# Performance work log

Hardware: AMD Instinct MI355X
Metric: run time of the kernel (lower is better)

Reference implementation:

```python
import jax, jax.numpy as jnp
import numpy as np
from jax import lax

# sign binarization to {-1,+1} with straight-through estimator (standard BNN binarizePM1)
@jax.custom_vjp
def binarize(x):
    return jnp.where(x >= 0, 1.0, -1.0).astype(x.dtype)

def _bin_fwd(x):
    return binarize(x), None

def _bin_bwd(_, g):
    return (g,)  # straight-through

binarize.defvjp(_bin_fwd, _bin_bwd)

def conv2d(x, w, b):
    # NCHW, OIHW, 3x3, stride 1, pad 1
    y = lax.conv_general_dilated(x, w, window_strides=(1, 1), padding=((1, 1), (1, 1)),
                                 dimension_numbers=('NCHW', 'OIHW', 'NCHW'))
    return y + b[None, :, None, None]

def maxpool2(x):
    return lax.reduce_window(x, -jnp.inf, lax.max, (1, 1, 2, 2), (1, 1, 2, 2), 'VALID')

def bn(x, gamma, beta, mean, var, eps=1e-5):
    # inference-mode batchnorm; broadcasts over channel axis 1 (4D) or feature axis 1 (2D)
    if x.ndim == 4:
        shp = (1, -1, 1, 1)
    else:
        shp = (1, -1)
    inv = gamma * lax.rsqrt(var + eps)
    return x * inv.reshape(shp) + (beta - mean * inv).reshape(shp)

def setup_inputs() -> dict:
    key = jax.random.key(0)
    ks = jax.random.split(key, 16)
    B = 4096
    d = {}
    d['x'] = jax.random.normal(ks[0], (B, 1, 28, 28), jnp.float32)
    d['conv1_w'] = jax.random.normal(ks[1], (64, 1, 3, 3), jnp.float32) * 0.1
    d['conv1_b'] = jax.random.normal(ks[2], (64,), jnp.float32) * 0.01
    d['conv2_w'] = jax.random.normal(ks[3], (64, 64, 3, 3), jnp.float32) * 0.05
    d['conv2_b'] = jax.random.normal(ks[4], (64,), jnp.float32) * 0.01
    d['fc1_w'] = jax.random.normal(ks[5], (2048, 7 * 7 * 64), jnp.float32) * 0.02
    d['fc1_b'] = jax.random.normal(ks[6], (2048,), jnp.float32) * 0.01
    d['fc2_w'] = jax.random.normal(ks[7], (10, 2048), jnp.float32) * 0.02
    d['fc2_b'] = jax.random.normal(ks[8], (10,), jnp.float32) * 0.01
    for i, (name, c) in enumerate([('bn1', 64), ('bn2', 64), ('bn3', 2048)]):
        d[name + '_gamma'] = jnp.ones((c,), jnp.float32)
        d[name + '_beta'] = jnp.zeros((c,), jnp.float32)
        d[name + '_mean'] = jax.random.normal(ks[9 + i], (c,), jnp.float32) * 0.1
        d[name + '_var'] = jax.random.uniform(ks[12 + i], (c,), jnp.float32, 0.5, 1.5)
    d['scale'] = jnp.array([1e-5], jnp.float32)
    return d

def reference(x, conv1_w, conv1_b, conv2_w, conv2_b, fc1_w, fc1_b, fc2_w, fc2_b,
              bn1_gamma, bn1_beta, bn1_mean, bn1_var,
              bn2_gamma, bn2_beta, bn2_mean, bn2_var,
              bn3_gamma, bn3_beta, bn3_mean, bn3_var, scale):
    h = conv2d(x, binarize(conv1_w), conv1_b)          # [B,64,28,28]
    h = maxpool2(h)                                    # [B,64,14,14]
    h = bn(h, bn1_gamma, bn1_beta, bn1_mean, bn1_var)
    h = jnp.clip(h, -1.0, 1.0)                         # hardtanh
    h = binarize(h)                                    # qact1
    h = conv2d(h, binarize(conv2_w), conv2_b)          # [B,64,14,14]
    h = maxpool2(h)                                    # [B,64,7,7]
    h = bn(h, bn2_gamma, bn2_beta, bn2_mean, bn2_var)
    h = jnp.clip(h, -1.0, 1.0)
    h = binarize(h)
    h = h.reshape(h.shape[0], -1)                      # [B,3136]
    h = h @ binarize(fc1_w).T + fc1_b                  # [B,2048]
    h = bn(h, bn3_gamma, bn3_beta, bn3_mean, bn3_var)
    h = jnp.clip(h, -1.0, 1.0)
    h = binarize(h)
    h = h @ binarize(fc2_w).T + fc2_b                  # [B,10]
    return h * scale
```

## Files before the change

### kernel.cpp

```cpp
#include <hip/hip_runtime.h>
#include <stdint.h>

typedef unsigned long long ULL;

__global__ __launch_bounds__(256) void prep_small(const float* __restrict__ w1,
        const float* __restrict__ w2, const float* __restrict__ fc2w,
        float* __restrict__ sgn1, ULL* __restrict__ wb2, ULL* __restrict__ wbf2) {
    int wave = threadIdx.x >> 6, lane = threadIdx.x & 63;
    int W = blockIdx.x * 4 + wave;
    if (W < 576) {
        int co = W / 9, tap = W - co * 9;
        ULL wd = __ballot(w2[(co * 64 + lane) * 9 + tap] >= 0.f);
        if (lane == 0) wb2[W] = wd;
    } else if (W < 896) {
        int idx = W - 576;
        int n = idx >> 5, k = idx & 31;
        ULL wd = __ballot(fc2w[n * 2048 + k * 64 + lane] >= 0.f);
        if (lane == 0) wbf2[idx] = wd;
    } else if (W < 905) {
        int i = (W - 896) * 64 + lane;
        if (i < 576) sgn1[i] = (w1[i] >= 0.f) ? 1.f : -1.f;
    }
}

__global__ __launch_bounds__(256) void prep_pack_fc1(const float* __restrict__ fc1w,
                                                     ULL* __restrict__ wbT) {
    __shared__ float rows[4 * 3136];
    int t = threadIdx.x;
    const float* src = fc1w + (size_t)blockIdx.x * 4 * 3136;
    for (int i = t; i < 4 * 3136; i += 256) rows[i] = src[i];
    __syncthreads();
    int wave = t >> 6, lane = t & 63;
    int n = blockIdx.x * 4 + wave;
    const float* r = rows + wave * 3136 + lane * 49;
    for (int p = 0; p < 49; ++p) {
        ULL wd = __ballot(r[p] >= 0.f);
        if (lane == 0) wbT[p * 2048 + n] = wd;
    }
}

__global__ __launch_bounds__(448, 4) void k1_conv1(const float* __restrict__ x,
        const float* __restrict__ sgn1, const float* __restrict__ b1,
        const float* __restrict__ g, const float* __restrict__ be,
        const float* __restrict__ mu, const float* __restrict__ va,
        ULL* __restrict__ qact1) {
    __shared__ float limg[30 * 30];
    int b = blockIdx.x, t = threadIdx.x;
    int wave = t >> 6, lane = t & 63;
    for (int i = t; i < 900; i += 448) limg[i] = 0.f;
    __syncthreads();
    const float* xb = x + (size_t)b * 784;
    for (int i = t; i < 784; i += 448) {
        int y = i / 28, xx = i - y * 28;
        limg[(xx + 1) * 30 + (y + 1)] = xb[i];
    }
    float w[9];
    #pragma unroll
    for (int k = 0; k < 9; ++k) w[k] = sgn1[lane * 9 + k];
    double iv = (double)g[lane] / sqrt((double)va[lane] + 1e-5);
    double cd = (double)be[lane] - (double)mu[lane] * iv;
    double bd = (double)b1[lane];
    __syncthreads();

    #pragma unroll
    for (int rr = 0; rr < 2; ++rr) {
        int py = wave + rr * 7;
        const float* base = &limg[2 * py];
        #pragma unroll
        for (int px = 0; px < 14; ++px) {
            float a00 = 0.f, a01 = 0.f, a10 = 0.f, a11 = 0.f;
            #pragma unroll
            for (int ky = 0; ky < 3; ++ky) {
                #pragma unroll
                for (int kx = 0; kx < 3; ++kx) {
                    float sv = w[ky * 3 + kx];
                    a00 = fmaf(base[(2 * px + kx)     * 30 + ky],     sv, a00);
                    a01 = fmaf(base[(2 * px + kx + 1) * 30 + ky],     sv, a01);
                    a10 = fmaf(base[(2 * px + kx)     * 30 + ky + 1], sv, a10);
                    a11 = fmaf(base[(2 * px + kx + 1) * 30 + ky + 1], sv, a11);
                }
            }
            float m = fmaxf(fmaxf(a00, a01), fmaxf(a10, a11));
            double v  = (double)m + bd;
            double tt = v * iv + cd;
            ULL word = __ballot(tt >= 0.0);
            if (lane == 0) qact1[(size_t)b * 196 + py * 14 + px] = word;
        }
    }
}

__global__ __launch_bounds__(448, 4) void k2_conv2(const ULL* __restrict__ qact1,
        const ULL* __restrict__ wb2, const float* __restrict__ b2,
        const float* __restrict__ g, const float* __restrict__ be,
        const float* __restrict__ mu, const float* __restrict__ va,
        ULL* __restrict__ qact2) {
    __shared__ ULL ap[16][16];
    int b = blockIdx.x, t = threadIdx.x;
    int pr = t >> 6, lane = t & 63;
    if (t < 256) ((ULL*)ap)[t] = 0ULL;
    __syncthreads();
    if (t < 196) ap[1 + t / 14][1 + t % 14] = qact1[(size_t)b * 196 + t];

    ULL wk[9];
    #pragma unroll
    for (int k = 0; k < 9; ++k) wk[k] = wb2[lane * 9 + k];
    int pw[9];
    #pragma unroll
    for (int k = 0; k < 9; ++k) pw[k] = 64 - 2 * (int)__popcll(wk[k]);

    double iv   = (double)g[lane] / sqrt((double)va[lane] + 1e-5);
    double cc   = (double)be[lane] - (double)mu[lane] * iv;
    double bias = (double)b2[lane];
    int am, thr;
    if (iv > 0.0) {
        double t0 = -cc / iv - bias;
        int c = (t0 < -590.0) ? -590 : (t0 > 590.0 ? 590 : (int)floor(t0) - 2);
        if (c < -590) c = -590;
        while (c <= 590 && !(((double)c + bias) * iv + cc >= 0.0)) ++c;
        am = 1; thr = c;
    } else if (iv < 0.0) {
        double t0 = -cc / iv - bias;
        int c = (t0 > 590.0) ? 590 : (t0 < -590.0 ? -590 : (int)ceil(t0) + 2);
        if (c > 590) c = 590;
        while (c >= -590 && !(((double)c + bias) * iv + cc >= 0.0)) --c;
        am = -1; thr = c;
    } else {
        am = 1; thr = (cc >= 0.0) ? -1000000 : 1000000;
    }
    int athr = am * thr;

    int corr[2][3];
    #pragma unroll
    for (int j = 0; j < 2; ++j) {
        bool tpad = (pr == 0 && j == 0);
        bool bpad = (pr == 6 && j == 1);
        #pragma unroll
        for (int cls = 0; cls < 3; ++cls) {
            int cacc = 0;
            #pragma unroll
            for (int r = 0; r < 3; ++r) {
                #pragma unroll
                for (int k = 0; k < 3; ++k) {
                    bool pad = (r == 0 && tpad) || (r == 2 && bpad) ||
                               (k == 0 && cls == 0) || (k == 2 && cls == 2);
                    if (pad) cacc += pw[r * 3 + k];
                }
            }
            corr[j][cls] = cacc;
        }
    }
    __syncthreads();

    const ULL* aprow = &ap[2 * pr][0];
    #pragma unroll
    for (int px = 0; px < 7; ++px) {
        int s00 = 0, s01 = 0, s10 = 0, s11 = 0;
        #pragma unroll
        for (int r = 0; r < 3; ++r) {
            #pragma unroll
            for (int k = 0; k < 3; ++k) {
                ULL w = wk[r * 3 + k];
                s00 += (int)__popcll(aprow[ r      * 16 + 2 * px + k    ] ^ w);
                s01 += (int)__popcll(aprow[ r      * 16 + 2 * px + k + 1] ^ w);
                s10 += (int)__popcll(aprow[(r + 1) * 16 + 2 * px + k    ] ^ w);
                s11 += (int)__popcll(aprow[(r + 1) * 16 + 2 * px + k + 1] ^ w);
            }
        }
        const int clsL = (px == 0) ? 0 : 1, clsR = (px == 6) ? 2 : 1;
        int d00 = 576 - 2 * s00 - corr[0][clsL];
        int d01 = 576 - 2 * s01 - corr[0][clsR];
        int d10 = 576 - 2 * s10 - corr[1][clsL];
        int d11 = 576 - 2 * s11 - corr[1][clsR];
        int m = max(max(d00, d01), max(d10, d11));
        ULL word = __ballot(am * m >= athr);
        if (lane == 0) qact2[(size_t)b * 49 + pr * 7 + px] = word;
    }
}

__global__ __launch_bounds__(256) void k3_fc1(const ULL* __restrict__ qact2,
        const ULL* __restrict__ wbT, const float* __restrict__ fb,
        const float* __restrict__ g, const float* __restrict__ be,
        const float* __restrict__ mu, const float* __restrict__ va,
        ULL* __restrict__ hbits) {
    __shared__ ULL xs[784];
    int t = threadIdx.x, wave = t >> 6, lane = t & 63;
    int b0 = blockIdx.x * 16;
    int gidx = blockIdx.y * 4 + wave;
    int n = gidx * 64 + lane;
    for (int i = t; i < 784; i += 256) xs[i] = qact2[(size_t)b0 * 49 + i];
    double iv   = (double)g[n] / sqrt((double)va[n] + 1e-5);
    double cc   = (double)be[n] - (double)mu[n] * iv;
    double bias = (double)fb[n];
    __syncthreads();
    int acc[16];
    #pragma unroll
    for (int i = 0; i < 16; ++i) acc[i] = 0;
    for (int p = 0; p < 49; ++p) {
        ULL w = wbT[p * 2048 + n];
        #pragma unroll
        for (int i = 0; i < 16; ++i)
            acc[i] += (int)__popcll(xs[i * 49 + p] ^ w);
    }
    #pragma unroll
    for (int i = 0; i < 16; ++i) {
        int dot = 3136 - 2 * acc[i];
        double tt = ((double)dot + bias) * iv + cc;
        ULL word = __ballot(tt >= 0.0);
        if (lane == 0) hbits[(size_t)(b0 + i) * 32 + gidx] = word;
    }
}

__global__ __launch_bounds__(256) void k4_fc2(const ULL* __restrict__ hbits,
        const ULL* __restrict__ wbf2, const float* __restrict__ b2,
        const float* __restrict__ scale, float* __restrict__ out, int total) {
    int gid = blockIdx.x * 256 + threadIdx.x;
    if (gid >= total) return;
    int b = gid / 10, n = gid - b * 10;
    const ULL* h = hbits + (size_t)b * 32;
    const ULL* w = wbf2 + n * 32;
    int acc = 0;
    #pragma unroll
    for (int k = 0; k < 32; ++k) acc += (int)__popcll(h[k] ^ w[k]);
    int dot = 2048 - 2 * acc;
    double v = ((double)dot + (double)b2[n]) * (double)scale[0];
    out[gid] = (float)v;
}

extern "C" void kernel_launch(void* const* d_in, const int* in_sizes, int n_in,
                              void* d_out, int out_size, void* d_ws, size_t ws_size,
                              hipStream_t stream) {
    const float* x      = (const float*)d_in[0];
    const float* w1     = (const float*)d_in[1];
    const float* b1     = (const float*)d_in[2];
    const float* w2     = (const float*)d_in[3];
    const float* b2     = (const float*)d_in[4];
    const float* fc1w   = (const float*)d_in[5];
    const float* fc1b   = (const float*)d_in[6];
    const float* fc2w   = (const float*)d_in[7];
    const float* fc2b   = (const float*)d_in[8];
    const float* g1 = (const float*)d_in[9],  *be1 = (const float*)d_in[10],
               *mu1 = (const float*)d_in[11], *va1 = (const float*)d_in[12];
    const float* g2 = (const float*)d_in[13], *be2 = (const float*)d_in[14],
               *mu2 = (const float*)d_in[15], *va2 = (const float*)d_in[16];
    const float* g3 = (const float*)d_in[17], *be3 = (const float*)d_in[18],
               *mu3 = (const float*)d_in[19], *va3 = (const float*)d_in[20];
    const float* scale = (const float*)d_in[21];
    float* out = (float*)d_out;

    int B = in_sizes[0] / 784;

    char* ws = (char*)d_ws;
    ULL* qact1 = (ULL*)(ws);
    ULL* qact2 = (ULL*)(ws + (size_t)B * 196 * 8);
    ULL* hbits = (ULL*)(ws + (size_t)B * 245 * 8);
    char* wsw  = ws + (size_t)B * 277 * 8;
    ULL* wb2   = (ULL*)(wsw);
    ULL* wbT   = (ULL*)(wsw + 576 * 8);
    ULL* wbf2  = (ULL*)(wsw + 576 * 8 + 49 * 2048 * 8);
    float* sgn1 = (float*)(wsw + 576 * 8 + 49 * 2048 * 8 + 320 * 8);

    prep_small<<<227, 256, 0, stream>>>(w1, w2, fc2w, sgn1, wb2, wbf2);
    prep_pack_fc1<<<512, 256, 0, stream>>>(fc1w, wbT);

    k1_conv1<<<B, 448, 0, stream>>>(x, sgn1, b1, g1, be1, mu1, va1, qact1);
    k2_conv2<<<B, 448, 0, stream>>>(qact1, wb2, b2, g2, be2, mu2, va2, qact2);
    k3_fc1<<<dim3(B / 16, 8), 256, 0, stream>>>(qact2, wbT, fc1b, g3, be3, mu3, va3, hbits);
    int total = B * 10;
    k4_fc2<<<(total + 255) / 256, 256, 0, stream>>>(hbits, wbf2, fc2b, scale, out, total);
}
```

Baseline: 314.2 us.

## Drop LDS staging in conv2; each wave streams its activation window in registers

The binary conv2 kernel no longer stages each sample's 14x14 activation words in shared memory behind two block barriers. Each wave now owns one (sample, output-row) pair and keeps a sliding 4x4 register window of activation words, loading two new columns per output pixel straight from global memory. The launch is regridded to 256-thread blocks covering B*7 waves. This removes LDS traffic and barriers, but every lane issues redundant global loads of the same words, and the new grid assumes B*7 is divisible by 4.

```diff
diff --git a/kernel.cpp b/kernel.cpp
--- a/kernel.cpp
+++ b/kernel.cpp
@@ -89,17 +89,14 @@
     }
 }
 
-__global__ __launch_bounds__(448, 4) void k2_conv2(const ULL* __restrict__ qact1,
+__global__ __launch_bounds__(256, 1) void k2_conv2(const ULL* __restrict__ qact1,
         const ULL* __restrict__ wb2, const float* __restrict__ b2,
         const float* __restrict__ g, const float* __restrict__ be,
         const float* __restrict__ mu, const float* __restrict__ va,
         ULL* __restrict__ qact2) {
-    __shared__ ULL ap[16][16];
-    int b = blockIdx.x, t = threadIdx.x;
-    int pr = t >> 6, lane = t & 63;
-    if (t < 256) ((ULL*)ap)[t] = 0ULL;
-    __syncthreads();
-    if (t < 196) ap[1 + t / 14][1 + t % 14] = qact1[(size_t)b * 196 + t];
+    int lane = threadIdx.x & 63;
+    int wid = blockIdx.x * 4 + (threadIdx.x >> 6);
+    int s = wid / 7, pr = wid - s * 7;
 
     ULL wk[9];
     #pragma unroll
@@ -149,21 +146,34 @@
             corr[j][cls] = cacc;
         }
     }
-    __syncthreads();
-
-    const ULL* aprow = &ap[2 * pr][0];
+
+    const ULL* base = qact1 + (size_t)s * 196;
+    int r0 = 2 * pr;
+    bool top = (pr > 0), bot = (pr < 6);
+
+    ULL cw[4][4];
+    #pragma unroll
+    for (int r = 0; r < 4; ++r) cw[0][r] = 0ULL;
+    #pragma unroll
+    for (int c = 0; c < 3; ++c) {
+        cw[c + 1][0] = top ? base[(r0 - 1) * 14 + c] : 0ULL;
+        cw[c + 1][1] = base[(r0    ) * 14 + c];
+        cw[c + 1][2] = base[(r0 + 1) * 14 + c];
+        cw[c + 1][3] = bot ? base[(r0 + 2) * 14 + c] : 0ULL;
+    }
+
     #pragma unroll
     for (int px = 0; px < 7; ++px) {
         int s00 = 0, s01 = 0, s10 = 0, s11 = 0;
         #pragma unroll
-        for (int r = 0; r < 3; ++r) {
-            #pragma unroll
-            for (int k = 0; k < 3; ++k) {
-                ULL w = wk[r * 3 + k];
-                s00 += (int)__popcll(aprow[ r      * 16 + 2 * px + k    ] ^ w);
-                s01 += (int)__popcll(aprow[ r      * 16 + 2 * px + k + 1] ^ w);
-                s10 += (int)__popcll(aprow[(r + 1) * 16 + 2 * px + k    ] ^ w);
-                s11 += (int)__popcll(aprow[(r + 1) * 16 + 2 * px + k + 1] ^ w);
+        for (int ky = 0; ky < 3; ++ky) {
+            #pragma unroll
+            for (int kx = 0; kx < 3; ++kx) {
+                ULL w = wk[ky * 3 + kx];
+                s00 += (int)__popcll(cw[kx    ][ky    ] ^ w);
+                s01 += (int)__popcll(cw[kx + 1][ky    ] ^ w);
+                s10 += (int)__popcll(cw[kx    ][ky + 1] ^ w);
+                s11 += (int)__popcll(cw[kx + 1][ky + 1] ^ w);
             }
         }
         const int clsL = (px == 0) ? 0 : 1, clsR = (px == 6) ? 2 : 1;
@@ -173,7 +183,24 @@
         int d11 = 576 - 2 * s11 - corr[1][clsR];
         int m = max(max(d00, d01), max(d10, d11));
         ULL word = __ballot(am * m >= athr);
-        if (lane == 0) qact2[(size_t)b * 49 + pr * 7 + px] = word;
+        if (lane == 0) qact2[(size_t)s * 49 + pr * 7 + px] = word;
+        if (px < 6) {
+            #pragma unroll
+            for (int r = 0; r < 4; ++r) { cw[0][r] = cw[2][r]; cw[1][r] = cw[3][r]; }
+            #pragma unroll
+            for (int c = 0; c < 2; ++c) {
+                const int col = 2 * px + 3 + c;
+                if (col <= 13) {
+                    cw[2 + c][0] = top ? base[(r0 - 1) * 14 + col] : 0ULL;
+                    cw[2 + c][1] = base[(r0    ) * 14 + col];
+                    cw[2 + c][2] = base[(r0 + 1) * 14 + col];
+                    cw[2 + c][3] = bot ? base[(r0 + 2) * 14 + col] : 0ULL;
+                } else {
+                    cw[2 + c][0] = 0ULL; cw[2 + c][1] = 0ULL;
+                    cw[2 + c][2] = 0ULL; cw[2 + c][3] = 0ULL;
+                }
+            }
+        }
     }
 }
 
@@ -263,7 +290,7 @@
     prep_pack_fc1<<<512, 256, 0, stream>>>(fc1w, wbT);
 
     k1_conv1<<<B, 448, 0, stream>>>(x, sgn1, b1, g1, be1, mu1, va1, qact1);
-    k2_conv2<<<B, 448, 0, stream>>>(qact1, wb2, b2, g2, be2, mu2, va2, qact2);
+    k2_conv2<<<B * 7 / 4, 256, 0, stream>>>(qact1, wb2, b2, g2, be2, mu2, va2, qact2);
     k3_fc1<<<dim3(B / 16, 8), 256, 0, stream>>>(qact2, wbT, fc1b, g3, be3, mu3, va3, hbits);
     int total = B * 10;
     k4_fc2<<<(total + 255) / 256, 256, 0, stream>>>(hbits, wbf2, fc2b, scale, out, total);
```

After: 306.3 us. 1.03x faster.
